# Kernel optimization log

Measured on AMD Instinct MI355X. Metric: run time of the kernel, lower is better.

## Reference

```python
import jax, jax.numpy as jnp
import numpy as np

NUM_HEADS = 16
EPS = 1e-5
CHUNK = 128  # chunk length for the chunked recurrent-state scan


def _linear_attention(x, Wq, Wk, Wv, Wo, bo):
    B, T, E = x.shape
    H = NUM_HEADS
    d = E // H

    def proj(W):
        # nn.Linear(bias=False): y = x @ W.T ; split heads -> (B,H,T,d)
        return (x @ W.T).reshape(B, T, H, d).transpose(0, 2, 1, 3)

    phi_q = jax.nn.elu(proj(Wq)) + 1.0
    phi_k = jax.nn.elu(proj(Wk)) + 1.0
    V = proj(Wv)

    nC = T // CHUNK
    # (nC, B, H, C, d) so lax.scan iterates over chunks of time
    def to_chunks(a):
        return a.reshape(B, H, nC, CHUNK, d).transpose(2, 0, 1, 3, 4)

    qc, kc, vc = to_chunks(phi_q), to_chunks(phi_k), to_chunks(V)
    mask = jnp.tril(jnp.ones((CHUNK, CHUNK), x.dtype))  # causal incl. diagonal

    S0 = jnp.zeros((B, H, d, d), x.dtype)  # running sum of k v^T
    z0 = jnp.zeros((B, H, d), x.dtype)     # running sum of phi_k

    def step(carry, inp):
        S, z = carry
        q, k, v = inp  # (B,H,C,d)
        A = jnp.einsum('bhid,bhjd->bhij', q, k) * mask
        num = jnp.einsum('bhij,bhjd->bhid', A, v) + jnp.einsum('bhid,bhde->bhie', q, S)
        den = jnp.sum(A, axis=-1) + jnp.einsum('bhid,bhd->bhi', q, z) + EPS
        out = num / den[..., None]
        S = S + jnp.einsum('bhjd,bhje->bhde', k, v)
        z = z + jnp.sum(k, axis=2)
        return (S, z), out

    _, outs = jax.lax.scan(step, (S0, z0), (qc, kc, vc))  # (nC,B,H,C,d)
    out = outs.transpose(1, 2, 0, 3, 4).reshape(B, H, T, d)
    out = out.transpose(0, 2, 1, 3).reshape(B, T, E)
    # out_proj (dropout p=0 / eval -> identity)
    return out @ Wo.T + bo


def setup_inputs() -> dict:
    key = jax.random.key(0)
    ks = jax.random.split(key, 6)
    B, T, E = 2, 2048, 1024
    s = 1.0 / np.sqrt(E)
    return {
        'x': jax.random.normal(ks[0], (B, T, E), jnp.float32),
        'Wq': jax.random.normal(ks[1], (E, E), jnp.float32) * s,
        'Wk': jax.random.normal(ks[2], (E, E), jnp.float32) * s,
        'Wv': jax.random.normal(ks[3], (E, E), jnp.float32) * s,
        'Wo': jax.random.normal(ks[4], (E, E), jnp.float32) * s,
        'bo': jnp.zeros((E,), jnp.float32),
    }


def reference(x, Wq, Wk, Wv, Wo, bo):
    return _linear_attention(x, Wq, Wk, Wv, Wo, bo)
```

## Files before the change

kernel.cpp:

```cpp
#include <hip/hip_runtime.h>
#include <hip/hip_bf16.h>
#include <stdint.h>

typedef __attribute__((ext_vector_type(4)))  float  floatx4;
typedef __attribute__((ext_vector_type(8)))  short  short8;
typedef __attribute__((ext_vector_type(8)))  unsigned short ushortx8;
typedef __attribute__((ext_vector_type(4)))  unsigned short ushortx4;

#define B_  2
#define T_  2048
#define E_  1024
#define H_  16
#define D_  64
#define C_  128
#define NC_ 16
#define M_  4096
#define EPS_ 1e-5f

__device__ __forceinline__ unsigned short f2b(float f) {
    union { float f; unsigned int u; } v; v.f = f;
    unsigned int r = v.u + 0x7fffu + ((v.u >> 16) & 1u);
    return (unsigned short)(r >> 16);
}
__device__ __forceinline__ float b2f(unsigned short b) {
    union { unsigned int u; float f; } v; v.u = ((unsigned int)b) << 16;
    return v.f;
}

__device__ __forceinline__ int stage_seg(int i) { return (i & 3) ^ ((i >> 3) & 3); }
__device__ __forceinline__ int frag_slot(int lane) {
    int m = lane & 15, q = lane >> 4;
    return m * 4 + (q ^ ((m >> 1) & 3));
}

__global__ __launch_bounds__(256) void convert_all(const float* __restrict__ x,
                                                   const float* __restrict__ Wq,
                                                   const float* __restrict__ Wk,
                                                   const float* __restrict__ Wv,
                                                   const float* __restrict__ Wo,
                                                   unsigned short* __restrict__ dst) {
    int i = (blockIdx.x * 256 + threadIdx.x) * 4;
    const float* s; int off;
    if (i < M_ * E_) { s = x; off = i; }
    else {
        int j = i - M_ * E_;
        int which = j >> 20;
        s = (which == 0) ? Wq : (which == 1) ? Wk : (which == 2) ? Wv : Wo;
        off = j & ((1 << 20) - 1);
    }
    float4 f = *(const float4*)(s + off);
    ushortx4 o;
    o[0] = f2b(f.x); o[1] = f2b(f.y); o[2] = f2b(f.z); o[3] = f2b(f.w);
    *(ushortx4*)(dst + i) = o;
}

__global__ __launch_bounds__(256) void gemm_qkv(const unsigned short* __restrict__ A,
                                                const unsigned short* __restrict__ Bm,
                                                unsigned short* __restrict__ Cb) {
    const int N = 3 * E_, K = E_;
    __shared__ __align__(16) unsigned short smem[12288];
    unsigned short* at = smem;
    unsigned short* bt = smem + 4096;
    int tid = threadIdx.x;
    int wave = tid >> 6, lane = tid & 63;
    int wr = wave >> 1, wc = wave & 1;
    int m = lane & 15, q = lane >> 4;
    int srow = lane >> 2, sseg = stage_seg(lane);
    int fs = frag_slot(lane);
    int row0 = blockIdx.y * 64, col0 = blockIdx.x * 128;
    floatx4 acc[2][4];
    for (int i = 0; i < 2; i++) for (int j = 0; j < 4; j++) acc[i][j] = floatx4{0.f, 0.f, 0.f, 0.f};

    for (int k0 = 0; k0 < K; k0 += 64) {
        __syncthreads();
        for (int p = 0; p < 2; p++) {
            int t = p * 4 + wave;
            const unsigned short* ga = A + (size_t)(row0 + (t & 3) * 16 + srow) * K + k0 + (t >> 2) * 32 + sseg * 8;
            __builtin_amdgcn_global_load_lds((const __attribute__((address_space(1))) unsigned int*)ga,
                (__attribute__((address_space(3))) unsigned int*)(at + t * 512), 16, 0, 0);
        }
        for (int p = 0; p < 4; p++) {
            int u = p * 4 + wave;
            const unsigned short* gb = Bm + (size_t)(col0 + (u & 7) * 16 + srow) * K + k0 + (u >> 3) * 32 + sseg * 8;
            __builtin_amdgcn_global_load_lds((const __attribute__((address_space(1))) unsigned int*)gb,
                (__attribute__((address_space(3))) unsigned int*)(bt + u * 512), 16, 0, 0);
        }
        __syncthreads();
        for (int kh = 0; kh < 2; kh++) {
            short8 af[2], bf[4];
            for (int mi = 0; mi < 2; mi++) af[mi] = *(const short8*)(at + (kh * 4 + wr * 2 + mi) * 512 + fs * 8);
            for (int ni = 0; ni < 4; ni++) bf[ni] = *(const short8*)(bt + (kh * 8 + wc * 4 + ni) * 512 + fs * 8);
            for (int mi = 0; mi < 2; mi++)
                for (int ni = 0; ni < 4; ni++)
                    acc[mi][ni] = __builtin_amdgcn_mfma_f32_16x16x32_bf16(af[mi], bf[ni], acc[mi][ni], 0, 0, 0);
        }
    }

    __syncthreads();
    unsigned short* epi = smem + wave * 2176;
    bool isphi = (col0 < 2 * E_);
    for (int mi = 0; mi < 2; mi++)
        for (int ni = 0; ni < 4; ni++)
            for (int reg = 0; reg < 4; reg++) {
                int lr = mi * 16 + q * 4 + reg;
                float v = acc[mi][ni][reg];
                if (isphi) v = (v > 0.f) ? (v + 1.f) : __expf(v);
                epi[lr * 68 + ni * 16 + m] = f2b(v);
            }
    for (int i = 0; i < 4; i++) {
        int s = i * 64 + lane;
        int lr = s >> 3, seg = s & 7;
        const unsigned short* p = epi + lr * 68 + seg * 8;
        ushortx4 lo = *(const ushortx4*)(p);
        ushortx4 hi = *(const ushortx4*)(p + 4);
        ushortx8 val;
        for (int e = 0; e < 4; e++) { val[e] = lo[e]; val[e + 4] = hi[e]; }
        int row = row0 + wr * 32 + lr;
        int col = col0 + wc * 64 + seg * 8;
        *(ushortx8*)(Cb + (size_t)row * N + col) = val;
    }
}

__global__ __launch_bounds__(256) void gemm_out(const unsigned short* __restrict__ A,
                                                const unsigned short* __restrict__ Bm,
                                                const float* __restrict__ bias,
                                                float* __restrict__ Cf) {
    const int N = E_, K = E_;
    __shared__ __align__(16) unsigned short at[8 * 512];
    __shared__ __align__(16) unsigned short bt[8 * 512];
    int tid = threadIdx.x;
    int wave = tid >> 6, lane = tid & 63;
    int wr = wave >> 1, wc = wave & 1;
    int m = lane & 15, q = lane >> 4;
    int srow = lane >> 2, sseg = stage_seg(lane);
    int fs = frag_slot(lane);
    int row0 = blockIdx.y * 64, col0 = blockIdx.x * 64;
    floatx4 acc[2][2];
    for (int i = 0; i < 2; i++) for (int j = 0; j < 2; j++) acc[i][j] = floatx4{0.f, 0.f, 0.f, 0.f};

    for (int k0 = 0; k0 < K; k0 += 64) {
        __syncthreads();
        for (int p = 0; p < 2; p++) {
            int t = p * 4 + wave;
            int rt = t & 3, kh = t >> 2;
            const unsigned short* ga = A  + (size_t)(row0 + rt * 16 + srow) * K + k0 + kh * 32 + sseg * 8;
            const unsigned short* gb = Bm + (size_t)(col0 + rt * 16 + srow) * K + k0 + kh * 32 + sseg * 8;
            __builtin_amdgcn_global_load_lds((const __attribute__((address_space(1))) unsigned int*)ga,
                (__attribute__((address_space(3))) unsigned int*)(at + t * 512), 16, 0, 0);
            __builtin_amdgcn_global_load_lds((const __attribute__((address_space(1))) unsigned int*)gb,
                (__attribute__((address_space(3))) unsigned int*)(bt + t * 512), 16, 0, 0);
        }
        __syncthreads();
        for (int kh = 0; kh < 2; kh++) {
            short8 af[2], bf[2];
            for (int mi = 0; mi < 2; mi++) af[mi] = *(const short8*)(at + (kh * 4 + wr * 2 + mi) * 512 + fs * 8);
            for (int ci = 0; ci < 2; ci++) bf[ci] = *(const short8*)(bt + (kh * 4 + wc * 2 + ci) * 512 + fs * 8);
            for (int mi = 0; mi < 2; mi++)
                for (int ci = 0; ci < 2; ci++)
                    acc[mi][ci] = __builtin_amdgcn_mfma_f32_16x16x32_bf16(af[mi], bf[ci], acc[mi][ci], 0, 0, 0);
        }
    }
    int qrow = q * 4;
    for (int ci = 0; ci < 2; ci++) {
        int col = col0 + wc * 32 + ci * 16 + m;
        float bv = bias[col];
        for (int mi = 0; mi < 2; mi++)
            for (int r2 = 0; r2 < 4; r2++) {
                int row = row0 + wr * 32 + mi * 16 + qrow + r2;
                Cf[(size_t)row * N + col] = acc[mi][ci][r2] + bv;
            }
    }
}

__global__ __launch_bounds__(256) void chunk_sums(const unsigned short* __restrict__ qkv,
                                                  float* __restrict__ Sc, float* __restrict__ zc) {
    int c = blockIdx.x, h = blockIdx.y, bb = blockIdx.z;
    __shared__ __align__(16) unsigned short Kt[64 * 132];
    __shared__ __align__(16) unsigned short Vt[80 * 132];
    int tid = threadIdx.x;
    int lane = tid & 63, w = tid >> 6;
    size_t rowb = (size_t)bb * T_ + (size_t)c * C_;
    int kcol = E_ + h * D_, vcol = 2 * E_ + h * D_;

    {
        int r4 = (tid >> 3) * 4;
        int seg = (tid & 7) * 8;
        ushortx8 kv[4], vv[4];
        for (int t = 0; t < 4; t++) {
            size_t g = (rowb + r4 + t) * 3072;
            kv[t] = *(const ushortx8*)(qkv + g + kcol + seg);
            vv[t] = *(const ushortx8*)(qkv + g + vcol + seg);
        }
        for (int e = 0; e < 8; e++) {
            ushortx4 ka, va;
            for (int t = 0; t < 4; t++) { ka[t] = kv[t][e]; va[t] = vv[t][e]; }
            *(ushortx4*)(Kt + (seg + e) * 132 + r4) = ka;
            *(ushortx4*)(Vt + (seg + e) * 132 + r4) = va;
        }
    }
    if (tid < 128) Vt[64 * 132 + tid] = 0x3f80;
    __syncthreads();

    floatx4 acc[5];
    for (int ni = 0; ni < 5; ni++) acc[ni] = floatx4{0.f, 0.f, 0.f, 0.f};
    int lm = lane & 15, lk = (lane >> 4) * 8;
    for (int k0 = 0; k0 < 128; k0 += 32) {
        short8 af = *(const short8*)(Kt + (w * 16 + lm) * 132 + k0 + lk);
        for (int ni = 0; ni < 5; ni++) {
            short8 bf = *(const short8*)(Vt + (ni * 16 + lm) * 132 + k0 + lk);
            acc[ni] = __builtin_amdgcn_mfma_f32_16x16x32_bf16(af, bf, acc[ni], 0, 0, 0);
        }
    }
    size_t base = ((size_t)(bb * H_ + h) * NC_ + c) * (size_t)(D_ * D_);
    int r0 = w * 16 + (lane >> 4) * 4;
    for (int ni = 0; ni < 4; ni++)
        for (int reg = 0; reg < 4; reg++)
            Sc[base + (size_t)(r0 + reg) * D_ + ni * 16 + lm] = acc[ni][reg];
    if (lm == 0) {
        size_t zb = ((size_t)(bb * H_ + h) * NC_ + c) * D_;
        for (int reg = 0; reg < 4; reg++) zc[zb + r0 + reg] = acc[4][reg];
    }
}

__global__ __launch_bounds__(256) void attn_kernel(const unsigned short* __restrict__ qkv,
                                                   const float* __restrict__ Sc,
                                                   const float* __restrict__ zc,
                                                   unsigned short* __restrict__ attn) {
    int c = blockIdx.x, h = blockIdx.y, bb = blockIdx.z;
    __shared__ __align__(16) unsigned short qs[128 * 68];
    __shared__ __align__(16) unsigned short ks[128 * 68];
    __shared__ __align__(16) unsigned short vt[64 * 132];
    __shared__ __align__(16) unsigned short ovl[128 * 36];
    __shared__ float zsh[64];
    int tid = threadIdx.x;
    int lane = tid & 63, w = tid >> 6;
    int lm = lane & 15, lq = lane >> 4;
    size_t rowb = (size_t)bb * T_ + (size_t)c * C_;
    int qcol = h * D_, kcol = E_ + h * D_, vcol = 2 * E_ + h * D_;

    for (int s = 0; s < 4; s++) {
        int off = s * 256 + tid;
        int r = off >> 3, seg = (off & 7) * 8;
        size_t g = (rowb + r) * 3072;
        ushortx8 q8 = *(const ushortx8*)(qkv + g + qcol + seg);
        ushortx8 k8 = *(const ushortx8*)(qkv + g + kcol + seg);
        *(ushortx8*)(qs + r * 68 + seg) = q8;
        *(ushortx8*)(ks + r * 68 + seg) = k8;
    }
    {
        int r4 = (tid >> 3) * 4;
        int seg = (tid & 7) * 8;
        ushortx8 vv[4];
        for (int t = 0; t < 4; t++)
            vv[t] = *(const ushortx8*)(qkv + (rowb + r4 + t) * 3072 + vcol + seg);
        for (int e = 0; e < 8; e++) {
            ushortx4 va;
            for (int t = 0; t < 4; t++) va[t] = vv[t][e];
            *(ushortx4*)(vt + (seg + e) * 132 + r4) = va;
        }
    }
    {
        size_t scb = ((size_t)(bb * H_ + h) * NC_) * (size_t)(D_ * D_);
        int p = tid * 16;
        float a[16];
        for (int i = 0; i < 16; i++) a[i] = 0.f;
        for (int j = 0; j < c; j++) {
            const float* Sj = Sc + scb + (size_t)j * (D_ * D_) + p;
            for (int q = 0; q < 16; q += 4) {
                float4 f = *(const float4*)(Sj + q);
                a[q] += f.x; a[q + 1] += f.y; a[q + 2] += f.z; a[q + 3] += f.w;
            }
        }
        for (int i = 0; i < 16; i++) {
            int d = (p + i) >> 6, e = (p + i) & 63;
            ovl[e * 68 + d] = f2b(a[i]);
        }
    }
    if (tid < 64) {
        size_t zb = ((size_t)(bb * H_ + h) * NC_) * D_;
        float zr = 0.f;
        for (int j = 0; j < c; j++) zr += zc[zb + (size_t)j * D_ + tid];
        zsh[tid] = zr;
    }
    __syncthreads();

    floatx4 acc[2][4];
    for (int mi = 0; mi < 2; mi++) for (int ni = 0; ni < 4; ni++) acc[mi][ni] = floatx4{0.f, 0.f, 0.f, 0.f};
    for (int k0 = 0; k0 < 64; k0 += 32) {
        short8 aq[2];
        for (int mi = 0; mi < 2; mi++)
            aq[mi] = *(const short8*)(qs + (w * 32 + mi * 16 + lm) * 68 + k0 + lq * 8);
        for (int ni = 0; ni < 4; ni++) {
            short8 bs = *(const short8*)(ovl + (ni * 16 + lm) * 68 + k0 + lq * 8);
            for (int mi = 0; mi < 2; mi++)
                acc[mi][ni] = __builtin_amdgcn_mfma_f32_16x16x32_bf16(aq[mi], bs, acc[mi][ni], 0, 0, 0);
        }
    }
    float dsum[2][4];
    {
        int d0 = lm * 4;
        float4 z4 = *(const float4*)(zsh + d0);
        for (int mi = 0; mi < 2; mi++)
            for (int reg = 0; reg < 4; reg++) {
                int row = w * 32 + mi * 16 + lq * 4 + reg;
                ushortx4 q4 = *(const ushortx4*)(qs + row * 68 + d0);
                dsum[mi][reg] = b2f(q4[0]) * z4.x + b2f(q4[1]) * z4.y + b2f(q4[2]) * z4.z + b2f(q4[3]) * z4.w;
            }
    }
    __syncthreads();

    for (int jt = 0; jt <= w; jt++) {
        floatx4 pa[2][2];
        for (int mi = 0; mi < 2; mi++) for (int ct = 0; ct < 2; ct++) pa[mi][ct] = floatx4{0.f, 0.f, 0.f, 0.f};
        for (int k0 = 0; k0 < 64; k0 += 32) {
            short8 aq[2];
            for (int mi = 0; mi < 2; mi++)
                aq[mi] = *(const short8*)(qs + (w * 32 + mi * 16 + lm) * 68 + k0 + lq * 8);
            for (int ct = 0; ct < 2; ct++) {
                short8 bk = *(const short8*)(ks + (jt * 32 + ct * 16 + lm) * 68 + k0 + lq * 8);
                for (int mi = 0; mi < 2; mi++)
                    pa[mi][ct] = __builtin_amdgcn_mfma_f32_16x16x32_bf16(aq[mi], bk, pa[mi][ct], 0, 0, 0);
            }
        }
        bool diag = (jt == w);
        for (int mi = 0; mi < 2; mi++)
            for (int ct = 0; ct < 2; ct++)
                for (int reg = 0; reg < 4; reg++) {
                    int il = mi * 16 + lq * 4 + reg;
                    int jl = ct * 16 + lm;
                    float v = pa[mi][ct][reg];
                    if (diag && jl > il) v = 0.f;
                    dsum[mi][reg] += v;
                    ovl[(w * 32 + il) * 36 + jl] = f2b(v);
                }
        short8 ap[2];
        for (int mi = 0; mi < 2; mi++)
            ap[mi] = *(const short8*)(ovl + (w * 32 + mi * 16 + lm) * 36 + lq * 8);
        for (int ni = 0; ni < 4; ni++) {
            short8 bv = *(const short8*)(vt + (ni * 16 + lm) * 132 + jt * 32 + lq * 8);
            for (int mi = 0; mi < 2; mi++)
                acc[mi][ni] = __builtin_amdgcn_mfma_f32_16x16x32_bf16(ap[mi], bv, acc[mi][ni], 0, 0, 0);
        }
    }

    for (int off = 1; off < 16; off <<= 1)
        for (int mi = 0; mi < 2; mi++)
            for (int reg = 0; reg < 4; reg++)
                dsum[mi][reg] += __shfl_xor(dsum[mi][reg], off);

    for (int mi = 0; mi < 2; mi++)
        for (int reg = 0; reg < 4; reg++) {
            float inv = 1.f / (dsum[mi][reg] + EPS_);
            int row = w * 32 + mi * 16 + lq * 4 + reg;
            for (int ni = 0; ni < 4; ni++)
                attn[(rowb + row) * E_ + h * D_ + ni * 16 + lm] = f2b(acc[mi][ni][reg] * inv);
        }
}

extern "C" void kernel_launch(void* const* d_in, const int* in_sizes, int n_in,
                              void* d_out, int out_size, void* d_ws, size_t ws_size,
                              hipStream_t stream) {
    const float* x  = (const float*)d_in[0];
    const float* Wq = (const float*)d_in[1];
    const float* Wk = (const float*)d_in[2];
    const float* Wv = (const float*)d_in[3];
    const float* Wo = (const float*)d_in[4];
    const float* bo = (const float*)d_in[5];
    float* out = (float*)d_out;

    const size_t MB = 1024 * 1024;
    uint8_t* ws = (uint8_t*)d_ws;
    unsigned short* xb    = (unsigned short*)(ws + 0);
    unsigned short* wb    = (unsigned short*)(ws + 8 * MB);
    unsigned short* wob   = wb + 3 * E_ * E_;
    unsigned short* qkvb  = (unsigned short*)(ws + 16 * MB);
    float* Sc = (float*)(ws + 40 * MB);
    float* zc = (float*)(ws + 48 * MB);
    unsigned short* attnb = xb;

    convert_all<<<(M_ * E_ + 4 * E_ * E_) / 1024, 256, 0, stream>>>(x, Wq, Wk, Wv, Wo, xb);

    gemm_qkv<<<dim3(24, 64), 256, 0, stream>>>(xb, wb, qkvb);
    chunk_sums<<<dim3(NC_, H_, B_), 256, 0, stream>>>(qkvb, Sc, zc);
    attn_kernel<<<dim3(NC_, H_, B_), 256, 0, stream>>>(qkvb, Sc, zc, attnb);
    gemm_out<<<dim3(16, 64), 256, 0, stream>>>(attnb, wob, bo, out);
}
```

Before: 165.6 us.

## Keep Q fragments in registers and compute q·z denominator via MFMA

Drops the Q shared-memory tile and loads each wave's Q MFMA fragments straight from global memory into registers, where they are reused for the inter-chunk state product and every intra-chunk score tile. The scalar q·z denominator loop is replaced by an extra MFMA against a zero-padded z row packed into the reused ovl buffer, and zsh is removed. Shared memory per block shrinks, which may raise occupancy, but more registers are held live and z is now rounded to bf16, which can reduce denominator precision.

```diff
diff --git a/kernel.cpp b/kernel.cpp
--- a/kernel.cpp
+++ b/kernel.cpp
@@ -227,11 +227,9 @@
                                                    const float* __restrict__ zc,
                                                    unsigned short* __restrict__ attn) {
     int c = blockIdx.x, h = blockIdx.y, bb = blockIdx.z;
-    __shared__ __align__(16) unsigned short qs[128 * 68];
     __shared__ __align__(16) unsigned short ks[128 * 68];
     __shared__ __align__(16) unsigned short vt[64 * 132];
-    __shared__ __align__(16) unsigned short ovl[128 * 36];
-    __shared__ float zsh[64];
+    __shared__ __align__(16) unsigned short ovl[80 * 68];
     int tid = threadIdx.x;
     int lane = tid & 63, w = tid >> 6;
     int lm = lane & 15, lq = lane >> 4;
@@ -241,10 +239,7 @@
     for (int s = 0; s < 4; s++) {
         int off = s * 256 + tid;
         int r = off >> 3, seg = (off & 7) * 8;
-        size_t g = (rowb + r) * 3072;
-        ushortx8 q8 = *(const ushortx8*)(qkv + g + qcol + seg);
-        ushortx8 k8 = *(const ushortx8*)(qkv + g + kcol + seg);
-        *(ushortx8*)(qs + r * 68 + seg) = q8;
+        ushortx8 k8 = *(const ushortx8*)(qkv + (rowb + r) * 3072 + kcol + seg);
         *(ushortx8*)(ks + r * 68 + seg) = k8;
     }
     {
@@ -280,46 +275,50 @@
         size_t zb = ((size_t)(bb * H_ + h) * NC_) * D_;
         float zr = 0.f;
         for (int j = 0; j < c; j++) zr += zc[zb + (size_t)j * D_ + tid];
-        zsh[tid] = zr;
-    }
+        ovl[64 * 68 + tid] = f2b(zr);
+        ovl[64 * 68 + 64 + (tid & 3)] = 0;
+    }
+    {
+        int idx = tid * 4;
+        if (idx < 1020)
+            for (int e = 0; e < 4; e++) ovl[65 * 68 + idx + e] = 0;
+    }
+    short8 aq[2][2];
+    for (int mi = 0; mi < 2; mi++)
+        for (int kk = 0; kk < 2; kk++)
+            aq[mi][kk] = *(const short8*)(qkv + (rowb + w * 32 + mi * 16 + lm) * 3072 + qcol + kk * 32 + lq * 8);
     __syncthreads();
 
-    floatx4 acc[2][4];
-    for (int mi = 0; mi < 2; mi++) for (int ni = 0; ni < 4; ni++) acc[mi][ni] = floatx4{0.f, 0.f, 0.f, 0.f};
-    for (int k0 = 0; k0 < 64; k0 += 32) {
-        short8 aq[2];
-        for (int mi = 0; mi < 2; mi++)
-            aq[mi] = *(const short8*)(qs + (w * 32 + mi * 16 + lm) * 68 + k0 + lq * 8);
+    floatx4 acc[2][4], dacc[2];
+    for (int mi = 0; mi < 2; mi++) {
+        for (int ni = 0; ni < 4; ni++) acc[mi][ni] = floatx4{0.f, 0.f, 0.f, 0.f};
+        dacc[mi] = floatx4{0.f, 0.f, 0.f, 0.f};
+    }
+    for (int kk = 0; kk < 2; kk++) {
+        int k0 = kk * 32;
         for (int ni = 0; ni < 4; ni++) {
             short8 bs = *(const short8*)(ovl + (ni * 16 + lm) * 68 + k0 + lq * 8);
             for (int mi = 0; mi < 2; mi++)
-                acc[mi][ni] = __builtin_amdgcn_mfma_f32_16x16x32_bf16(aq[mi], bs, acc[mi][ni], 0, 0, 0);
-        }
+                acc[mi][ni] = __builtin_amdgcn_mfma_f32_16x16x32_bf16(aq[mi][kk], bs, acc[mi][ni], 0, 0, 0);
+        }
+        short8 bz = *(const short8*)(ovl + (64 + lm) * 68 + k0 + lq * 8);
+        for (int mi = 0; mi < 2; mi++)
+            dacc[mi] = __builtin_amdgcn_mfma_f32_16x16x32_bf16(aq[mi][kk], bz, dacc[mi], 0, 0, 0);
     }
     float dsum[2][4];
-    {
-        int d0 = lm * 4;
-        float4 z4 = *(const float4*)(zsh + d0);
-        for (int mi = 0; mi < 2; mi++)
-            for (int reg = 0; reg < 4; reg++) {
-                int row = w * 32 + mi * 16 + lq * 4 + reg;
-                ushortx4 q4 = *(const ushortx4*)(qs + row * 68 + d0);
-                dsum[mi][reg] = b2f(q4[0]) * z4.x + b2f(q4[1]) * z4.y + b2f(q4[2]) * z4.z + b2f(q4[3]) * z4.w;
-            }
-    }
+    for (int mi = 0; mi < 2; mi++)
+        for (int reg = 0; reg < 4; reg++) dsum[mi][reg] = dacc[mi][reg];
     __syncthreads();
 
     for (int jt = 0; jt <= w; jt++) {
         floatx4 pa[2][2];
         for (int mi = 0; mi < 2; mi++) for (int ct = 0; ct < 2; ct++) pa[mi][ct] = floatx4{0.f, 0.f, 0.f, 0.f};
-        for (int k0 = 0; k0 < 64; k0 += 32) {
-            short8 aq[2];
-            for (int mi = 0; mi < 2; mi++)
-                aq[mi] = *(const short8*)(qs + (w * 32 + mi * 16 + lm) * 68 + k0 + lq * 8);
+        for (int kk = 0; kk < 2; kk++) {
+            int k0 = kk * 32;
             for (int ct = 0; ct < 2; ct++) {
                 short8 bk = *(const short8*)(ks + (jt * 32 + ct * 16 + lm) * 68 + k0 + lq * 8);
                 for (int mi = 0; mi < 2; mi++)
-                    pa[mi][ct] = __builtin_amdgcn_mfma_f32_16x16x32_bf16(aq[mi], bk, pa[mi][ct], 0, 0, 0);
+                    pa[mi][ct] = __builtin_amdgcn_mfma_f32_16x16x32_bf16(aq[mi][kk], bk, pa[mi][ct], 0, 0, 0);
             }
         }
         bool diag = (jt == w);
```

Measured after the change: 167.2 us. Within noise of the previous version (+0.9%).
